# Performance work log

Measured on AMD Instinct MI355X. Metric: run time of the kernel, lower is better.

The kernel has to match this reference:

```python
import jax, jax.numpy as jnp
import numpy as np

N, E, G = 25600, 409600, 128   # nodes, edges, graphs
IN, H, C = 200, 4, 64          # raw feat dim, heads, hidden_channels
IN2 = 2 * IN                   # after NaN-mask concat
BN_EPS = 1e-5

def _glorot(key, shape):
    lim = float(np.sqrt(6.0 / (shape[0] + shape[-1])))
    return jax.random.uniform(key, shape, jnp.float32, -lim, lim)

def setup_inputs():
    key = jax.random.key(0)
    k = iter(jax.random.split(key, 40))
    inp = {
        "x": jax.random.normal(next(k), (N, IN), jnp.float32),
        "edge_index": jax.random.randint(next(k), (2, E), 0, N, jnp.int32),
        "edge_attr": jax.random.normal(next(k), (E, 1), jnp.float32),
        "batch": jnp.repeat(jnp.arange(G, dtype=jnp.int32), N // G),
    }
    dims = [(IN2, H, C), (H * C, H, C), (H * C, 1, C)]
    for i, (din, h, c) in enumerate(dims):
        inp[f"W{i}"] = _glorot(next(k), (din, h * c))
        inp[f"as{i}"] = _glorot(next(k), (h, c))
        inp[f"ad{i}"] = _glorot(next(k), (h, c))
        inp[f"We{i}"] = _glorot(next(k), (1, h * c))
        inp[f"ae{i}"] = _glorot(next(k), (h, c))
        inp[f"b{i}"] = jnp.zeros((h * c,), jnp.float32)
    inp["bn_g"] = jnp.ones((H * C,), jnp.float32)
    inp["bn_b"] = jnp.zeros((H * C,), jnp.float32)
    inp["bn_m"] = jnp.zeros((H * C,), jnp.float32)
    inp["bn_v"] = jnp.ones((H * C,), jnp.float32)
    inp["cw1"] = _glorot(next(k), (C, C))
    inp["cb1"] = jnp.zeros((C,), jnp.float32)
    inp["cw2"] = _glorot(next(k), (C, 2))
    inp["cb2"] = jnp.zeros((2,), jnp.float32)
    return inp

def _gat(x, src, dst, ea, W, att_s, att_d, We, att_e, b, heads, ch):
    """PyG GATConv (edge_dim=1, add_self_loops=True, fill_value='mean', concat=True)."""
    n = x.shape[0]
    # self-loop edge_attr = mean of incoming edge_attr per destination node
    cnt = jax.ops.segment_sum(jnp.ones((ea.shape[0], 1), ea.dtype), dst, n)
    loop_ea = jax.ops.segment_sum(ea, dst, n) / jnp.maximum(cnt, 1.0)
    idx = jnp.arange(n, dtype=src.dtype)
    src = jnp.concatenate([src, idx])
    dst = jnp.concatenate([dst, idx])
    ea = jnp.concatenate([ea, loop_ea], axis=0)
    h = (x @ W).reshape(n, heads, ch)                      # [N,H,C]
    a_s = jnp.einsum('nhc,hc->nh', h, att_s)
    a_d = jnp.einsum('nhc,hc->nh', h, att_d)
    a_e = jnp.einsum('ehc,hc->eh', (ea @ We).reshape(-1, heads, ch), att_e)
    alpha = jax.nn.leaky_relu(a_s[src] + a_d[dst] + a_e, 0.2)   # [E',H]
    # segment softmax over destination neighborhoods
    m = jax.ops.segment_max(alpha, dst, n)
    ex = jnp.exp(alpha - m[dst])
    z = jax.ops.segment_sum(ex, dst, n)
    alpha = ex / (z[dst] + 1e-16)
    out = jax.ops.segment_sum(h[src] * alpha[:, :, None], dst, n)  # [N,H,C]
    return out.reshape(n, heads * ch) + b

def reference(x, edge_index, edge_attr, batch,
              W0, as0, ad0, We0, ae0, b0,
              W1, as1, ad1, We1, ae1, b1,
              W2, as2, ad2, We2, ae2, b2,
              bn_g, bn_b, bn_m, bn_v, cw1, cb1, cw2, cb2):
    nan_mask = jnp.isnan(x).astype(x.dtype)
    x = jnp.concatenate([jnp.nan_to_num(x), nan_mask], axis=-1)   # [N, 2*IN]
    edge_attr = jnp.nan_to_num(edge_attr)
    src, dst = edge_index[0], edge_index[1]
    for (W, a_s, a_d, We, a_e, b) in [(W0, as0, ad0, We0, ae0, b0),
                                      (W1, as1, ad1, We1, ae1, b1)]:
        x = _gat(x, src, dst, edge_attr, W, a_s, a_d, We, a_e, b, H, C)
        x = (x - bn_m) / jnp.sqrt(bn_v + BN_EPS) * bn_g + bn_b    # eval-mode BN
        x = jax.nn.relu(x)                                        # dropout = identity (eval)
    x = _gat(x, src, dst, edge_attr, W2, as2, ad2, We2, ae2, b2, 1, C)
    # global mean pool over graphs
    cnt = jax.ops.segment_sum(jnp.ones((x.shape[0], 1), x.dtype), batch, G)
    g = jax.ops.segment_sum(x, batch, G) / jnp.maximum(cnt, 1.0)  # [G, C]
    hdn = jax.nn.gelu(g @ cw1 + cb1, approximate=False)
    return hdn @ cw2 + cb2                                        # [G, 2]
```

## Files before the change

kernel.cpp:

```cpp
#include <hip/hip_runtime.h>
#include <hip/hip_bf16.h>

static const int kN  = 25600;
static const int kE  = 409600;
static const int kG  = 128;
static const int kNPG = 200;
static const int kIN = 200;
static const int kIN2 = 400;
#define BN_EPS_ 1e-5f

typedef __attribute__((ext_vector_type(8))) short short8;
typedef __attribute__((ext_vector_type(4))) float f32x4;

__device__ __forceinline__ float bu(ushort u) {
  union { float f; unsigned u32; } x; x.u32 = ((unsigned)u) << 16; return x.f;
}
__device__ __forceinline__ ushort f2u(float v) {
  __hip_bfloat16 t = __float2bfloat16(v);
  return *(ushort*)&t;
}

__device__ __forceinline__ float wredSum(float v) {
#pragma unroll
  for (int off = 1; off < 64; off <<= 1) v += __shfl_xor(v, off, 64);
  return v;
}

__device__ __forceinline__ float lrelu(float a) { return (a > 0.f) ? a : 0.2f * a; }

__global__ void k_zero(unsigned int* __restrict__ p, int n) {
  int i = blockIdx.x * blockDim.x + threadIdx.x;
  if (i < n) p[i] = 0u;
}


__global__ void k_prep_x(const float* __restrict__ x, ushort* __restrict__ x2) {
  int i = blockIdx.x * blockDim.x + threadIdx.x;
  if (i >= kN * kIN) return;
  int n = i / kIN, j = i - n * kIN;
  float v = x[i];
  bool bad = (v != v);
  x2[(size_t)n * kIN2 + j] = f2u(bad ? 0.f : v);
  x2[(size_t)n * kIN2 + kIN + j] = f2u(bad ? 1.f : 0.f);
}

__global__ void k_prep_wt(const float* __restrict__ W, ushort* __restrict__ Wt,
                          int K, int N) {
  int i = blockIdx.x * blockDim.x + threadIdx.x;
  if (i >= K * N) return;
  int n = i / K, k = i - n * K;
  Wt[(size_t)n * K + k] = f2u(W[(size_t)k * N + n]);
}

__global__ void k_wedot_all(const float* __restrict__ We0, const float* __restrict__ ae0,
                            const float* __restrict__ We1, const float* __restrict__ ae1,
                            const float* __restrict__ We2, const float* __restrict__ ae2,
                            float* __restrict__ wed) {
  int b = blockIdx.x, tid = threadIdx.x;
  const float* We = (b == 0) ? We0 : (b == 1) ? We1 : We2;
  const float* ae = (b == 0) ? ae0 : (b == 1) ? ae1 : ae2;
  int n = (b == 2) ? 64 : 256;
  float v = (tid < n) ? We[tid] * ae[tid] : 0.f;
  v = wredSum(v);
  if ((tid & 63) == 0 && tid < n) wed[b * 4 + (tid >> 6)] = v;
}

__global__ void k_edge_cnt(const int* __restrict__ ei, int* __restrict__ deg,
                           int* __restrict__ epos) {
  int e = blockIdx.x * blockDim.x + threadIdx.x;
  if (e >= kE) return;
  epos[e] = atomicAdd(&deg[ei[kE + e]], 1);
}

__global__ void k_scan_chunk(const int* __restrict__ deg, int* __restrict__ rowp,
                             int* __restrict__ csum) {
  __shared__ int s[1024];
  int tid = threadIdx.x;
  int i = blockIdx.x * 1024 + tid;
  int v = deg[i];
  s[tid] = v;
  __syncthreads();
  for (int off = 1; off < 1024; off <<= 1) {
    int t = (tid >= off) ? s[tid - off] : 0;
    __syncthreads();
    s[tid] += t;
    __syncthreads();
  }
  rowp[i] = s[tid] - v;
  if (tid == 1023) csum[blockIdx.x] = s[tid];
}

__global__ void k_scan_sums(const int* __restrict__ csum, int* __restrict__ coff, int nchunk) {
  if (threadIdx.x == 0 && blockIdx.x == 0) {
    int acc = 0;
    for (int i = 0; i < nchunk; i++) { coff[i] = acc; acc += csum[i]; }
  }
}

__global__ void k_scan_fix(int* __restrict__ rowp, const int* __restrict__ coff) {
  int i = blockIdx.x * blockDim.x + threadIdx.x;
  if (i >= kN) return;
  rowp[i] += coff[i >> 10];
}

__global__ void k_scatter_n(const int* __restrict__ ei, const float* __restrict__ ea,
                            const int* __restrict__ rowp, const int* __restrict__ epos,
                            int* __restrict__ esrc, float* __restrict__ eaC) {
  int e = blockIdx.x * blockDim.x + threadIdx.x;
  if (e >= kE) return;
  int d = ei[kE + e];
  int slot = rowp[d] + d + epos[e];
  esrc[slot] = ei[e];
  float v = ea[e];
  if (v != v) v = 0.f;
  eaC[slot] = v;
}

__global__ void k_selfloop(const int* __restrict__ rowp, const int* __restrict__ deg,
                           int* __restrict__ esrc, float* __restrict__ eaC) {
  int n = blockIdx.x * 4 + (threadIdx.x >> 6);
  int lane = threadIdx.x & 63;
  int start = rowp[n] + n;
  int dg = deg[n];
  float s = 0.f;
  for (int k = lane; k < dg; k += 64) s += eaC[start + k];
  s = wredSum(s);
  if (lane == 0) {
    esrc[start + dg] = n;
    eaC[start + dg] = s / fmaxf((float)dg, 1.f);
  }
}

#define GBK 64
#define GPAD 72

template <int BN>
__global__ __launch_bounds__(256) void k_gemm_f(const ushort* __restrict__ A,
                                                const ushort* __restrict__ Bt,
                                                ushort* __restrict__ C,
                                                const float* __restrict__ as_g,
                                                const float* __restrict__ ad_g,
                                                float* __restrict__ a_sg,
                                                float* __restrict__ a_dg, int K) {
  constexpr int MI = (BN == 256) ? 4 : 1;
  constexpr int H = (BN == 256) ? 4 : 1;
  __shared__ ushort As[64 * GPAD];
  __shared__ ushort Bs[BN * GPAD];
  int tid = threadIdx.x;
  int lane = tid & 63, w = tid >> 6;
  int l15 = lane & 15, l4 = lane >> 4;
  int row0 = blockIdx.y * 64;
  int wr = (BN == 256) ? 0 : (w * 16);
  int wc = (BN == 256) ? (w * 64) : 0;
  f32x4 acc[MI][4] = {};

  int ach = tid & 7;
  int arow = tid >> 3;

  for (int kt = 0; kt < K; kt += GBK) {
    __syncthreads();
#pragma unroll
    for (int p = 0; p < 2; p++) {
      int r = p * 32 + arow;
      int kg = kt + ach * 8;
      short8 v = {0, 0, 0, 0, 0, 0, 0, 0};
      if (kg < K) v = *(const short8*)&A[(size_t)(row0 + r) * K + kg];
      *(short8*)&As[r * GPAD + ach * 8] = v;
    }
#pragma unroll
    for (int p = 0; p < BN / 32; p++) {
      int r = p * 32 + arow;
      int kg = kt + ach * 8;
      short8 v = {0, 0, 0, 0, 0, 0, 0, 0};
      if (kg < K) v = *(const short8*)&Bt[(size_t)r * K + kg];
      *(short8*)&Bs[r * GPAD + ach * 8] = v;
    }
    __syncthreads();
#pragma unroll
    for (int kk = 0; kk < 2; kk++) {
      short8 af[MI], bf[4];
#pragma unroll
      for (int mi = 0; mi < MI; mi++)
        af[mi] = *(const short8*)&As[(wr + mi * 16 + l15) * GPAD + kk * 32 + l4 * 8];
#pragma unroll
      for (int ni = 0; ni < 4; ni++)
        bf[ni] = *(const short8*)&Bs[(wc + ni * 16 + l15) * GPAD + kk * 32 + l4 * 8];
#pragma unroll
      for (int mi = 0; mi < MI; mi++)
#pragma unroll
        for (int ni = 0; ni < 4; ni++)
          acc[mi][ni] = __builtin_amdgcn_mfma_f32_16x16x32_bf16(af[mi], bf[ni],
                                                                acc[mi][ni], 0, 0, 0);
    }
  }
#pragma unroll
  for (int mi = 0; mi < MI; mi++) {
    int rbase = row0 + wr + mi * 16 + l4 * 4;
#pragma unroll
    for (int ni = 0; ni < 4; ni++) {
      int col = wc + ni * 16 + l15;
#pragma unroll
      for (int r = 0; r < 4; r++)
        C[(size_t)(rbase + r) * BN + col] = f2u(acc[mi][ni][r]);
    }
  }
  float asv[4], adv[4];
#pragma unroll
  for (int ni = 0; ni < 4; ni++) {
    asv[ni] = as_g[wc + ni * 16 + l15];
    adv[ni] = ad_g[wc + ni * 16 + l15];
  }
  int hh = (BN == 256) ? w : 0;
#pragma unroll
  for (int mi = 0; mi < MI; mi++) {
#pragma unroll
    for (int r = 0; r < 4; r++) {
      float ps = 0.f, pd = 0.f;
#pragma unroll
      for (int ni = 0; ni < 4; ni++) {
        ps += acc[mi][ni][r] * asv[ni];
        pd += acc[mi][ni][r] * adv[ni];
      }
#pragma unroll
      for (int off = 1; off < 16; off <<= 1) {
        ps += __shfl_xor(ps, off, 64);
        pd += __shfl_xor(pd, off, 64);
      }
      if (l15 == 0) {
        int row = row0 + wr + mi * 16 + l4 * 4 + r;
        a_sg[row * H + hh] = ps;
        a_dg[row * H + hh] = pd;
      }
    }
  }
}

__global__ __launch_bounds__(256) void k_agg4(
    const ushort* __restrict__ hbuf, const int* __restrict__ rowp,
    const int* __restrict__ deg, const int* __restrict__ esrc,
    const float* __restrict__ eaC, const float* __restrict__ a_s,
    const float* __restrict__ a_d, const float* __restrict__ wed,
    const float* __restrict__ bias, const float* __restrict__ bng,
    const float* __restrict__ bnb, const float* __restrict__ bnm,
    const float* __restrict__ bnv, ushort* __restrict__ xout) {
  int tid = threadIdx.x;
  int w = tid >> 6, lane = tid & 63;
  int d = blockIdx.x * 4 + w;
  int start = rowp[d] + d;
  int total = deg[d] + 1;
  int h = lane >> 4;
  float adh = a_d[d * 4 + h];
  float wdh = wed[h];

  int c0 = lane * 4;
  float a0 = 0.f, a1 = 0.f, a2 = 0.f, a3 = 0.f, sz = 0.f;
  int k = 0;
  for (; k + 4 <= total; k += 4) {
    int s0 = esrc[start + k], s1 = esrc[start + k + 1];
    int s2 = esrc[start + k + 2], s3 = esrc[start + k + 3];
    float e0 = eaC[start + k], e1 = eaC[start + k + 1];
    float e2 = eaC[start + k + 2], e3 = eaC[start + k + 3];
    ushort4 v0 = *(const ushort4*)&hbuf[(size_t)s0 * 256 + c0];
    ushort4 v1 = *(const ushort4*)&hbuf[(size_t)s1 * 256 + c0];
    ushort4 v2 = *(const ushort4*)&hbuf[(size_t)s2 * 256 + c0];
    ushort4 v3 = *(const ushort4*)&hbuf[(size_t)s3 * 256 + c0];
    float w0 = __expf(lrelu(a_s[s0 * 4 + h] + adh + e0 * wdh));
    float w1 = __expf(lrelu(a_s[s1 * 4 + h] + adh + e1 * wdh));
    float w2 = __expf(lrelu(a_s[s2 * 4 + h] + adh + e2 * wdh));
    float w3 = __expf(lrelu(a_s[s3 * 4 + h] + adh + e3 * wdh));
    sz += (w0 + w1) + (w2 + w3);
    a0 += w0 * bu(v0.x) + w1 * bu(v1.x) + w2 * bu(v2.x) + w3 * bu(v3.x);
    a1 += w0 * bu(v0.y) + w1 * bu(v1.y) + w2 * bu(v2.y) + w3 * bu(v3.y);
    a2 += w0 * bu(v0.z) + w1 * bu(v1.z) + w2 * bu(v2.z) + w3 * bu(v3.z);
    a3 += w0 * bu(v0.w) + w1 * bu(v1.w) + w2 * bu(v2.w) + w3 * bu(v3.w);
  }
  for (; k < total; k++) {
    int s0 = esrc[start + k];
    float e0 = eaC[start + k];
    ushort4 v0 = *(const ushort4*)&hbuf[(size_t)s0 * 256 + c0];
    float w0 = __expf(lrelu(a_s[s0 * 4 + h] + adh + e0 * wdh));
    sz += w0;
    a0 += w0 * bu(v0.x); a1 += w0 * bu(v0.y);
    a2 += w0 * bu(v0.z); a3 += w0 * bu(v0.w);
  }
  float winv = 1.f / (sz + 1e-16f);
  a0 *= winv; a1 *= winv; a2 *= winv; a3 *= winv;

  float4 bi = *(const float4*)&bias[c0];
  a0 += bi.x; a1 += bi.y; a2 += bi.z; a3 += bi.w;
  float4 g4 = *(const float4*)&bng[c0], b4 = *(const float4*)&bnb[c0];
  float4 m4 = *(const float4*)&bnm[c0], v4 = *(const float4*)&bnv[c0];
  a0 = fmaxf((a0 - m4.x) * rsqrtf(v4.x + BN_EPS_) * g4.x + b4.x, 0.f);
  a1 = fmaxf((a1 - m4.y) * rsqrtf(v4.y + BN_EPS_) * g4.y + b4.y, 0.f);
  a2 = fmaxf((a2 - m4.z) * rsqrtf(v4.z + BN_EPS_) * g4.z + b4.z, 0.f);
  a3 = fmaxf((a3 - m4.w) * rsqrtf(v4.w + BN_EPS_) * g4.w + b4.w, 0.f);
  ushort4 o = make_ushort4(f2u(a0), f2u(a1), f2u(a2), f2u(a3));
  *(ushort4*)&xout[(size_t)d * 256 + c0] = o;
}

__global__ __launch_bounds__(256) void k_agg1(
    const ushort* __restrict__ hbuf, const int* __restrict__ rowp,
    const int* __restrict__ deg, const int* __restrict__ esrc,
    const float* __restrict__ eaC, const float* __restrict__ a_s,
    const float* __restrict__ a_d, const float* __restrict__ wed,
    const float* __restrict__ bias, float* __restrict__ xout) {
  int tid = threadIdx.x;
  int w = tid >> 6, lane = tid & 63;
  int d = blockIdx.x * 4 + w;
  int start = rowp[d] + d;
  int total = deg[d] + 1;
  float adh = a_d[d];
  float wdh = wed[0];

  float acc = 0.f, sz = 0.f;
  int k = 0;
  for (; k + 4 <= total; k += 4) {
    int s0 = esrc[start + k], s1 = esrc[start + k + 1];
    int s2 = esrc[start + k + 2], s3 = esrc[start + k + 3];
    float e0 = eaC[start + k], e1 = eaC[start + k + 1];
    float e2 = eaC[start + k + 2], e3 = eaC[start + k + 3];
    float v0 = bu(hbuf[(size_t)s0 * 64 + lane]);
    float v1 = bu(hbuf[(size_t)s1 * 64 + lane]);
    float v2 = bu(hbuf[(size_t)s2 * 64 + lane]);
    float v3 = bu(hbuf[(size_t)s3 * 64 + lane]);
    float w0 = __expf(lrelu(a_s[s0] + adh + e0 * wdh));
    float w1 = __expf(lrelu(a_s[s1] + adh + e1 * wdh));
    float w2 = __expf(lrelu(a_s[s2] + adh + e2 * wdh));
    float w3 = __expf(lrelu(a_s[s3] + adh + e3 * wdh));
    sz += (w0 + w1) + (w2 + w3);
    acc += w0 * v0 + w1 * v1 + w2 * v2 + w3 * v3;
  }
  for (; k < total; k++) {
    int s0 = esrc[start + k];
    float w0 = __expf(lrelu(a_s[s0] + adh + eaC[start + k] * wdh));
    sz += w0;
    acc += w0 * bu(hbuf[(size_t)s0 * 64 + lane]);
  }
  acc = acc / (sz + 1e-16f) + bias[lane];
  xout[(size_t)d * 64 + lane] = acc;
}

__global__ void k_poolhead(const float* __restrict__ xin,
                           const float* __restrict__ cw1, const float* __restrict__ cb1,
                           const float* __restrict__ cw2, const float* __restrict__ cb2,
                           float* __restrict__ out) {
  __shared__ float part[4][64];
  __shared__ float gb[64], hb[64];
  int g = blockIdx.x, tid = threadIdx.x;
  int c = tid & 63, w = tid >> 6;
  float acc = 0.f;
  size_t base = (size_t)g * kNPG * 64;
  for (int n = w; n < kNPG; n += 4) acc += xin[base + (size_t)n * 64 + c];
  part[w][c] = acc;
  __syncthreads();
  if (tid < 64) {
    float s = (part[0][c] + part[1][c]) + (part[2][c] + part[3][c]);
    gb[c] = s * (1.f / kNPG);
  }
  __syncthreads();
  if (tid < 64) {
    float s = cb1[c];
#pragma unroll 8
    for (int i = 0; i < 64; i++) s += gb[i] * cw1[i * 64 + c];
    s = 0.5f * s * (1.f + erff(s * 0.70710678118654752f));
    hb[c] = s;
  }
  __syncthreads();
  if (tid < 2) {
    float o = cb2[tid];
    for (int i = 0; i < 64; i++) o += hb[i] * cw2[i * 2 + tid];
    out[g * 2 + tid] = o;
  }
}


extern "C" void kernel_launch(void* const* d_in, const int* in_sizes, int n_in,
                              void* d_out, int out_size, void* d_ws, size_t ws_size,
                              hipStream_t stream) {
  (void)in_sizes; (void)n_in; (void)out_size; (void)ws_size;
  const float* x  = (const float*)d_in[0];
  const int* ei   = (const int*)d_in[1];
  const float* ea = (const float*)d_in[2];
  const float *W[3], *as_[3], *ad_[3], *We[3], *ae[3], *bi[3];
  for (int l = 0; l < 3; l++) {
    W[l]   = (const float*)d_in[4 + l * 6 + 0];
    as_[l] = (const float*)d_in[4 + l * 6 + 1];
    ad_[l] = (const float*)d_in[4 + l * 6 + 2];
    We[l]  = (const float*)d_in[4 + l * 6 + 3];
    ae[l]  = (const float*)d_in[4 + l * 6 + 4];
    bi[l]  = (const float*)d_in[4 + l * 6 + 5];
  }
  const float* bng = (const float*)d_in[22];
  const float* bnb = (const float*)d_in[23];
  const float* bnm = (const float*)d_in[24];
  const float* bnv = (const float*)d_in[25];
  const float* cw1 = (const float*)d_in[26];
  const float* cb1 = (const float*)d_in[27];
  const float* cw2 = (const float*)d_in[28];
  const float* cb2 = (const float*)d_in[29];

  char* p = (char*)d_ws;
  auto alloc = [&](size_t bytes) -> void* {
    void* r = (void*)p;
    p += (bytes + 255) & ~(size_t)255;
    return r;
  };
  ushort* x2b   = (ushort*)alloc((size_t)kN * kIN2 * 2);
  ushort* hbufb = (ushort*)alloc((size_t)kN * 256 * 2);
  ushort* xbA   = (ushort*)alloc((size_t)kN * 256 * 2);
  ushort* xbB   = (ushort*)alloc((size_t)kN * 256 * 2);
  float*  fbuf  = (float*)alloc((size_t)kN * 64 * 4);
  ushort* Wt0   = (ushort*)alloc((size_t)kIN2 * 256 * 2);
  ushort* Wt1   = (ushort*)alloc((size_t)256 * 256 * 2);
  ushort* Wt2   = (ushort*)alloc((size_t)256 * 64 * 2);
  float* a_s    = (float*)alloc((size_t)kN * 4 * 4);
  float* a_d    = (float*)alloc((size_t)kN * 4 * 4);
  int* rowp     = (int*)alloc((size_t)kN * 4);
  int* esrc     = (int*)alloc((size_t)(kE + kN) * 4);
  float* eaC    = (float*)alloc((size_t)(kE + kN) * 4);
  int* epos     = (int*)alloc((size_t)kE * 4);
  float* wed    = (float*)alloc(256);
  int* csum     = (int*)alloc(256);
  int* coff     = (int*)alloc(256);
  int* deg      = (int*)alloc((size_t)kN * 4);
  k_zero<<<(kN + 255) / 256, 256, 0, stream>>>((unsigned int*)deg, kN);

  k_prep_x<<<(kN * kIN + 255) / 256, 256, 0, stream>>>(x, x2b);
  k_prep_wt<<<(kIN2 * 256 + 255) / 256, 256, 0, stream>>>(W[0], Wt0, kIN2, 256);
  k_prep_wt<<<(256 * 256 + 255) / 256, 256, 0, stream>>>(W[1], Wt1, 256, 256);
  k_prep_wt<<<(256 * 64 + 255) / 256, 256, 0, stream>>>(W[2], Wt2, 256, 64);
  k_wedot_all<<<3, 256, 0, stream>>>(We[0], ae[0], We[1], ae[1], We[2], ae[2], wed);
  k_edge_cnt<<<(kE + 255) / 256, 256, 0, stream>>>(ei, deg, epos);
  k_scan_chunk<<<kN / 1024, 1024, 0, stream>>>(deg, rowp, csum);
  k_scan_sums<<<1, 64, 0, stream>>>(csum, coff, kN / 1024);
  k_scan_fix<<<(kN + 255) / 256, 256, 0, stream>>>(rowp, coff);
  k_scatter_n<<<(kE + 255) / 256, 256, 0, stream>>>(ei, ea, rowp, epos, esrc, eaC);
  k_selfloop<<<kN / 4, 256, 0, stream>>>(rowp, deg, esrc, eaC);

  int Kd[3] = {kIN2, 256, 256};
  const ushort* Ain[3] = {x2b, xbA, xbB};
  const ushort* Wt[3] = {Wt0, Wt1, Wt2};
  ushort* loutB[2] = {xbA, xbB};
  dim3 gg(1, kN / 64);

  for (int l = 0; l < 3; l++) {
    if (l < 2)
      k_gemm_f<256><<<gg, 256, 0, stream>>>(Ain[l], Wt[l], hbufb, as_[l], ad_[l],
                                            a_s, a_d, Kd[l]);
    else
      k_gemm_f<64><<<gg, 256, 0, stream>>>(Ain[l], Wt[l], hbufb, as_[l], ad_[l],
                                           a_s, a_d, Kd[l]);
    if (l < 2)
      k_agg4<<<kN / 4, 256, 0, stream>>>(hbufb, rowp, deg, esrc, eaC, a_s, a_d,
                                         &wed[l * 4], bi[l], bng, bnb, bnm, bnv,
                                         loutB[l]);
    else
      k_agg1<<<kN / 4, 256, 0, stream>>>(hbufb, rowp, deg, esrc, eaC, a_s, a_d,
                                         &wed[8], bi[l], fbuf);
  }

  k_poolhead<<<kG, 256, 0, stream>>>(fbuf, cw1, cb1, cw2, cb2, (float*)d_out);
}
```

Measured before the change: 344.6 us.

## Merge prep kernels, fold scan offsets, shrink GEMM tile, prefetch edge indices

Merges the three weight-transpose launches and the edge-weight dot kernel into one launch, and folds the serial chunk-offset scan into the fix-up kernel, which each block now computes itself. The first two GEMMs use a 32-row M tile instead of 64, which doubles the grid and may raise occupancy, though each block reuses the B tile less. The aggregation loops load the next group of source indices and edge attributes one iteration ahead, so the index loads overlap the feature gathers. Launch count and latency drop, at the cost of redundant csum summation per block and extra registers.

```diff
diff --git a/kernel.cpp b/kernel.cpp
--- a/kernel.cpp
+++ b/kernel.cpp
@@ -44,25 +44,36 @@
   x2[(size_t)n * kIN2 + kIN + j] = f2u(bad ? 1.f : 0.f);
 }
 
-__global__ void k_prep_wt(const float* __restrict__ W, ushort* __restrict__ Wt,
-                          int K, int N) {
-  int i = blockIdx.x * blockDim.x + threadIdx.x;
-  if (i >= K * N) return;
-  int n = i / K, k = i - n * K;
-  Wt[(size_t)n * K + k] = f2u(W[(size_t)k * N + n]);
-}
-
-__global__ void k_wedot_all(const float* __restrict__ We0, const float* __restrict__ ae0,
-                            const float* __restrict__ We1, const float* __restrict__ ae1,
-                            const float* __restrict__ We2, const float* __restrict__ ae2,
-                            float* __restrict__ wed) {
-  int b = blockIdx.x, tid = threadIdx.x;
-  const float* We = (b == 0) ? We0 : (b == 1) ? We1 : We2;
-  const float* ae = (b == 0) ? ae0 : (b == 1) ? ae1 : ae2;
-  int n = (b == 2) ? 64 : 256;
-  float v = (tid < n) ? We[tid] * ae[tid] : 0.f;
-  v = wredSum(v);
-  if ((tid & 63) == 0 && tid < n) wed[b * 4 + (tid >> 6)] = v;
+__global__ void k_prep_w(const float* __restrict__ W0, ushort* __restrict__ Wt0,
+                         const float* __restrict__ W1, ushort* __restrict__ Wt1,
+                         const float* __restrict__ W2, ushort* __restrict__ Wt2,
+                         const float* __restrict__ We0, const float* __restrict__ ae0,
+                         const float* __restrict__ We1, const float* __restrict__ ae1,
+                         const float* __restrict__ We2, const float* __restrict__ ae2,
+                         float* __restrict__ wed) {
+  if (blockIdx.x >= 720) {
+    int b = blockIdx.x - 720, tid = threadIdx.x;
+    const float* We = (b == 0) ? We0 : (b == 1) ? We1 : We2;
+    const float* ae = (b == 0) ? ae0 : (b == 1) ? ae1 : ae2;
+    int n = (b == 2) ? 64 : 256;
+    float v = (tid < n) ? We[tid] * ae[tid] : 0.f;
+    v = wredSum(v);
+    if ((tid & 63) == 0 && tid < n) wed[b * 4 + (tid >> 6)] = v;
+    return;
+  }
+  int i = blockIdx.x * 256 + threadIdx.x;
+  if (i < 102400) {
+    int n = i / kIN2, k = i - n * kIN2;
+    Wt0[(size_t)n * kIN2 + k] = f2u(W0[(size_t)k * 256 + n]);
+  } else if (i < 102400 + 65536) {
+    int j = i - 102400;
+    int n = j >> 8, k = j & 255;
+    Wt1[(size_t)n * 256 + k] = f2u(W1[(size_t)k * 256 + n]);
+  } else {
+    int j = i - 102400 - 65536;
+    int n = j >> 8, k = j & 255;
+    Wt2[(size_t)n * 256 + k] = f2u(W2[(size_t)k * 64 + n]);
+  }
 }
 
 __global__ void k_edge_cnt(const int* __restrict__ ei, int* __restrict__ deg,
@@ -90,17 +101,16 @@
   if (tid == 1023) csum[blockIdx.x] = s[tid];
 }
 
-__global__ void k_scan_sums(const int* __restrict__ csum, int* __restrict__ coff, int nchunk) {
-  if (threadIdx.x == 0 && blockIdx.x == 0) {
-    int acc = 0;
-    for (int i = 0; i < nchunk; i++) { coff[i] = acc; acc += csum[i]; }
-  }
-}
-
-__global__ void k_scan_fix(int* __restrict__ rowp, const int* __restrict__ coff) {
-  int i = blockIdx.x * blockDim.x + threadIdx.x;
-  if (i >= kN) return;
-  rowp[i] += coff[i >> 10];
+__global__ void k_scan_fix(int* __restrict__ rowp, const int* __restrict__ csum) {
+  __shared__ int off;
+  int i = blockIdx.x * 256 + threadIdx.x;
+  if (threadIdx.x == 0) {
+    int c = i >> 10, acc = 0;
+    for (int j = 0; j < c; j++) acc += csum[j];
+    off = acc;
+  }
+  __syncthreads();
+  rowp[i] += off;
 }
 
 __global__ void k_scatter_n(const int* __restrict__ ei, const float* __restrict__ ea,
@@ -134,7 +144,7 @@
 #define GBK 64
 #define GPAD 72
 
-template <int BN>
+template <int BN, int MT>
 __global__ __launch_bounds__(256) void k_gemm_f(const ushort* __restrict__ A,
                                                 const ushort* __restrict__ Bt,
                                                 ushort* __restrict__ C,
@@ -142,14 +152,14 @@
                                                 const float* __restrict__ ad_g,
                                                 float* __restrict__ a_sg,
                                                 float* __restrict__ a_dg, int K) {
-  constexpr int MI = (BN == 256) ? 4 : 1;
+  constexpr int MI = (BN == 256) ? (MT / 16) : 1;
   constexpr int H = (BN == 256) ? 4 : 1;
-  __shared__ ushort As[64 * GPAD];
+  __shared__ ushort As[MT * GPAD];
   __shared__ ushort Bs[BN * GPAD];
   int tid = threadIdx.x;
   int lane = tid & 63, w = tid >> 6;
   int l15 = lane & 15, l4 = lane >> 4;
-  int row0 = blockIdx.y * 64;
+  int row0 = blockIdx.y * MT;
   int wr = (BN == 256) ? 0 : (w * 16);
   int wc = (BN == 256) ? (w * 64) : 0;
   f32x4 acc[MI][4] = {};
@@ -160,7 +170,7 @@
   for (int kt = 0; kt < K; kt += GBK) {
     __syncthreads();
 #pragma unroll
-    for (int p = 0; p < 2; p++) {
+    for (int p = 0; p < MT / 32; p++) {
       int r = p * 32 + arow;
       int kg = kt + ach * 8;
       short8 v = {0, 0, 0, 0, 0, 0, 0, 0};
@@ -254,12 +264,25 @@
 
   int c0 = lane * 4;
   float a0 = 0.f, a1 = 0.f, a2 = 0.f, a3 = 0.f, sz = 0.f;
+  int ns0 = 0, ns1 = 0, ns2 = 0, ns3 = 0;
+  float ne0 = 0.f, ne1 = 0.f, ne2 = 0.f, ne3 = 0.f;
+  if (total >= 4) {
+    ns0 = esrc[start + 0]; ns1 = esrc[start + 1];
+    ns2 = esrc[start + 2]; ns3 = esrc[start + 3];
+    ne0 = eaC[start + 0]; ne1 = eaC[start + 1];
+    ne2 = eaC[start + 2]; ne3 = eaC[start + 3];
+  }
   int k = 0;
   for (; k + 4 <= total; k += 4) {
-    int s0 = esrc[start + k], s1 = esrc[start + k + 1];
-    int s2 = esrc[start + k + 2], s3 = esrc[start + k + 3];
-    float e0 = eaC[start + k], e1 = eaC[start + k + 1];
-    float e2 = eaC[start + k + 2], e3 = eaC[start + k + 3];
+    int s0 = ns0, s1 = ns1, s2 = ns2, s3 = ns3;
+    float e0 = ne0, e1 = ne1, e2 = ne2, e3 = ne3;
+    int kn = k + 4;
+    if (kn + 4 <= total) {
+      ns0 = esrc[start + kn + 0]; ns1 = esrc[start + kn + 1];
+      ns2 = esrc[start + kn + 2]; ns3 = esrc[start + kn + 3];
+      ne0 = eaC[start + kn + 0]; ne1 = eaC[start + kn + 1];
+      ne2 = eaC[start + kn + 2]; ne3 = eaC[start + kn + 3];
+    }
     ushort4 v0 = *(const ushort4*)&hbuf[(size_t)s0 * 256 + c0];
     ushort4 v1 = *(const ushort4*)&hbuf[(size_t)s1 * 256 + c0];
     ushort4 v2 = *(const ushort4*)&hbuf[(size_t)s2 * 256 + c0];
@@ -313,12 +336,25 @@
   float wdh = wed[0];
 
   float acc = 0.f, sz = 0.f;
+  int ns0 = 0, ns1 = 0, ns2 = 0, ns3 = 0;
+  float ne0 = 0.f, ne1 = 0.f, ne2 = 0.f, ne3 = 0.f;
+  if (total >= 4) {
+    ns0 = esrc[start + 0]; ns1 = esrc[start + 1];
+    ns2 = esrc[start + 2]; ns3 = esrc[start + 3];
+    ne0 = eaC[start + 0]; ne1 = eaC[start + 1];
+    ne2 = eaC[start + 2]; ne3 = eaC[start + 3];
+  }
   int k = 0;
   for (; k + 4 <= total; k += 4) {
-    int s0 = esrc[start + k], s1 = esrc[start + k + 1];
-    int s2 = esrc[start + k + 2], s3 = esrc[start + k + 3];
-    float e0 = eaC[start + k], e1 = eaC[start + k + 1];
-    float e2 = eaC[start + k + 2], e3 = eaC[start + k + 3];
+    int s0 = ns0, s1 = ns1, s2 = ns2, s3 = ns3;
+    float e0 = ne0, e1 = ne1, e2 = ne2, e3 = ne3;
+    int kn = k + 4;
+    if (kn + 4 <= total) {
+      ns0 = esrc[start + kn + 0]; ns1 = esrc[start + kn + 1];
+      ns2 = esrc[start + kn + 2]; ns3 = esrc[start + kn + 3];
+      ne0 = eaC[start + kn + 0]; ne1 = eaC[start + kn + 1];
+      ne2 = eaC[start + kn + 2]; ne3 = eaC[start + kn + 3];
+    }
     float v0 = bu(hbuf[(size_t)s0 * 64 + lane]);
     float v1 = bu(hbuf[(size_t)s1 * 64 + lane]);
     float v2 = bu(hbuf[(size_t)s2 * 64 + lane]);
@@ -421,19 +457,15 @@
   int* epos     = (int*)alloc((size_t)kE * 4);
   float* wed    = (float*)alloc(256);
   int* csum     = (int*)alloc(256);
-  int* coff     = (int*)alloc(256);
   int* deg      = (int*)alloc((size_t)kN * 4);
   k_zero<<<(kN + 255) / 256, 256, 0, stream>>>((unsigned int*)deg, kN);
 
   k_prep_x<<<(kN * kIN + 255) / 256, 256, 0, stream>>>(x, x2b);
-  k_prep_wt<<<(kIN2 * 256 + 255) / 256, 256, 0, stream>>>(W[0], Wt0, kIN2, 256);
-  k_prep_wt<<<(256 * 256 + 255) / 256, 256, 0, stream>>>(W[1], Wt1, 256, 256);
-  k_prep_wt<<<(256 * 64 + 255) / 256, 256, 0, stream>>>(W[2], Wt2, 256, 64);
-  k_wedot_all<<<3, 256, 0, stream>>>(We[0], ae[0], We[1], ae[1], We[2], ae[2], wed);
+  k_prep_w<<<723, 256, 0, stream>>>(W[0], Wt0, W[1], Wt1, W[2], Wt2,
+                                    We[0], ae[0], We[1], ae[1], We[2], ae[2], wed);
   k_edge_cnt<<<(kE + 255) / 256, 256, 0, stream>>>(ei, deg, epos);
   k_scan_chunk<<<kN / 1024, 1024, 0, stream>>>(deg, rowp, csum);
-  k_scan_sums<<<1, 64, 0, stream>>>(csum, coff, kN / 1024);
-  k_scan_fix<<<(kN + 255) / 256, 256, 0, stream>>>(rowp, coff);
+  k_scan_fix<<<kN / 256, 256, 0, stream>>>(rowp, csum);
   k_scatter_n<<<(kE + 255) / 256, 256, 0, stream>>>(ei, ea, rowp, epos, esrc, eaC);
   k_selfloop<<<kN / 4, 256, 0, stream>>>(rowp, deg, esrc, eaC);
 
@@ -441,15 +473,16 @@
   const ushort* Ain[3] = {x2b, xbA, xbB};
   const ushort* Wt[3] = {Wt0, Wt1, Wt2};
   ushort* loutB[2] = {xbA, xbB};
-  dim3 gg(1, kN / 64);
+  dim3 gg32(1, kN / 32);
+  dim3 gg64(1, kN / 64);
 
   for (int l = 0; l < 3; l++) {
     if (l < 2)
-      k_gemm_f<256><<<gg, 256, 0, stream>>>(Ain[l], Wt[l], hbufb, as_[l], ad_[l],
-                                            a_s, a_d, Kd[l]);
+      k_gemm_f<256, 32><<<gg32, 256, 0, stream>>>(Ain[l], Wt[l], hbufb, as_[l],
+                                                  ad_[l], a_s, a_d, Kd[l]);
     else
-      k_gemm_f<64><<<gg, 256, 0, stream>>>(Ain[l], Wt[l], hbufb, as_[l], ad_[l],
-                                           a_s, a_d, Kd[l]);
+      k_gemm_f<64, 64><<<gg64, 256, 0, stream>>>(Ain[l], Wt[l], hbufb, as_[l],
+                                                 ad_[l], a_s, a_d, Kd[l]);
     if (l < 2)
       k_agg4<<<kN / 4, 256, 0, stream>>>(hbufb, rowp, deg, esrc, eaC, a_s, a_d,
                                          &wed[l * 4], bi[l], bng, bnb, bnm, bnv,
```

Measured after the change: 344.2 us. Within noise of the previous version (-0.1%).
